# Optimization experiments

Measured on AMD Instinct MI355X. Metric: run time of the kernel, lower is better.

## Reference

```python
import jax, jax.numpy as jnp
import numpy as np

# ---- Cl(3,0) Cayley table: blade order [1, e1, e2, e3, e12, e13, e23, e123] ----
_IDX2BM = [0, 1, 2, 4, 3, 5, 6, 7]
_BM2IDX = {b: i for i, b in enumerate(_IDX2BM)}

def _blade_mul(i, j):
    a, b = _IDX2BM[i], _IDX2BM[j]
    s, aa = 0, a >> 1
    while aa:
        s += bin(aa & b).count('1')
        aa >>= 1
    return _BM2IDX[a ^ b], (-1) ** s

_pairs = [(i, j) + _blade_mul(i, j) for i in range(8) for j in range(8) if i != j]
_pairs = [(i, j, k, s) for (i, j, k, s) in _pairs if k != i and k != j]
SRC_I = np.array([p[0] for p in _pairs])  # (42,)
SRC_J = np.array([p[1] for p in _pairs])
TGT   = np.array([p[2] for p in _pairs])
SIGN  = np.array([p[3] for p in _pairs], dtype=np.float32)

ROPE_THETA = 10000.0


def _rope_tables(T, D, dtype):
    inv_freq = 1.0 / (ROPE_THETA ** (jnp.arange(0, D, 2, dtype=jnp.float32) / D))
    freqs = jnp.arange(T, dtype=jnp.float32)[:, None] * inv_freq[None, :]  # (T, D/2)
    emb = jnp.concatenate([freqs, freqs], axis=-1)  # (T, D)
    return jnp.cos(emb).astype(dtype), jnp.sin(emb).astype(dtype)


def _rotate_half(x):
    x1, x2 = jnp.split(x, 2, axis=-1)
    return jnp.concatenate([-x2, x1], axis=-1)


def setup_inputs() -> dict:
    key = jax.random.key(0)
    k1, k2, k3 = jax.random.split(key, 3)
    B, T, N, D = 2, 2048, 8, 128
    d_model = N * D
    mv = jax.random.normal(k1, (B, T, N, D), dtype=jnp.float32)
    # nn.Linear weights, stored as (in, out) for x @ W; scaled like default init
    W_qkv = jax.random.normal(k2, (d_model, 3 * d_model), dtype=jnp.float32) / np.sqrt(d_model)
    W_o = jax.random.normal(k3, (d_model, d_model), dtype=jnp.float32) / np.sqrt(d_model)
    alpha = jnp.ones((8, 8), dtype=jnp.float32) * 0.01  # cayley_mix_init_scale
    return {"mv": mv, "W_qkv": W_qkv, "W_o": W_o, "alpha": alpha}


def reference(mv, W_qkv, W_o, alpha):
    B, T, N, D = mv.shape
    x_flat = mv.reshape(B, T, N * D)
    qkv = (x_flat @ W_qkv).reshape(B, T, 3, N, D)
    q, k, v = qkv[:, :, 0], qkv[:, :, 1], qkv[:, :, 2]  # (B, T, N, D)

    cos, sin = _rope_tables(T, D, mv.dtype)  # (T, D)
    cos = cos[None, :, None, :]
    sin = sin[None, :, None, :]
    q = q * cos + _rotate_half(q) * sin
    k = k * cos + _rotate_half(k) * sin

    # (B, N, T, D)
    q = q.transpose(0, 2, 1, 3)
    k = k.transpose(0, 2, 1, 3)
    v = v.transpose(0, 2, 1, 3)

    scale = 1.0 / jnp.sqrt(jnp.asarray(D, dtype=mv.dtype))
    scores = jnp.einsum('bntd,bnsd->bnts', q, k) * scale  # (B, N, T, T)
    causal = jnp.tril(jnp.ones((T, T), dtype=bool))
    scores = jnp.where(causal[None, None], scores, -jnp.inf)
    attn = jax.nn.softmax(scores, axis=-1)
    out = jnp.einsum('bnts,bnsd->bntd', attn, v)  # (B, N, T, D)

    out = out.transpose(0, 2, 1, 3).reshape(B, T, N * D)
    out = (out @ W_o).reshape(B, T, N, D)

    # Cayley cross-blade mixing
    si, sj, tgt = jnp.asarray(SRC_I), jnp.asarray(SRC_J), jnp.asarray(TGT)
    pair_w = alpha[si, sj] * jnp.asarray(SIGN)  # (42,)
    contrib = out[:, :, si, :] * out[:, :, sj, :] * pair_w[None, None, :, None]
    mixed = jnp.zeros_like(out).at[:, :, tgt, :].add(contrib)
    return out + mixed
```

## Files before the change

kernel.cpp:

```cpp
#include <hip/hip_runtime.h>
#include <stdint.h>


typedef __attribute__((ext_vector_type(8)))  __bf16 bf16x8;
typedef __attribute__((ext_vector_type(8)))  uint16_t u16x8;
typedef __attribute__((ext_vector_type(4)))  float  f32x4;

__device__ __forceinline__ uint16_t f2bf(float f) {
    uint32_t u = __float_as_uint(f);
    u += 0x7FFFu + ((u >> 16) & 1u);
    return (uint16_t)(u >> 16);
}
__device__ __forceinline__ float bf2f(uint16_t h) {
    return __uint_as_float(((uint32_t)h) << 16);
}

__device__ __forceinline__ void gload_lds16(const void* g, void* l) {
    __builtin_amdgcn_global_load_lds(
        (__attribute__((address_space(1))) void*)g,
        (__attribute__((address_space(3))) void*)l, 16, 0, 0);
}

__global__ __launch_bounds__(256) void k_prep(const float* __restrict__ mv,
                                              const float* __restrict__ Wqkv,
                                              const float* __restrict__ Wo,
                                              uint16_t* __restrict__ Xbf,
                                              uint16_t* __restrict__ Wqt,
                                              uint16_t* __restrict__ Wot,
                                              float* __restrict__ ct,
                                              float* __restrict__ st) {
    __shared__ uint16_t tile[64][65];
    const int bid = blockIdx.x;
    const int tid = threadIdx.x;
    if (bid < 4096) {
        int i = bid * 256 + tid;
        float4 v = ((const float4*)mv)[i];
        ((ushort4*)Xbf)[i] = make_ushort4(f2bf(v.x), f2bf(v.y), f2bf(v.z), f2bf(v.w));
    } else if (bid < 5120) {
        const float* W; uint16_t* Wt; int N, bx, by;
        if (bid < 4864) { W = Wqkv; Wt = Wqt; N = 3072;
                          int b2 = bid - 4096; bx = b2 % 48; by = b2 / 48; }
        else            { W = Wo;   Wt = Wot; N = 1024;
                          int b3 = bid - 4864; bx = b3 & 15; by = b3 >> 4; }
        const int k0 = by * 64, n0 = bx * 64;
        const int c = tid & 63, r4 = tid >> 6;
#pragma unroll
        for (int i = 0; i < 16; ++i) {
            int r = r4 + i * 4;
            tile[r][c] = f2bf(W[(size_t)(k0 + r) * N + n0 + c]);
        }
        __syncthreads();
#pragma unroll
        for (int i = 0; i < 16; ++i) {
            int r = r4 + i * 4;
            Wt[(size_t)(n0 + r) * 1024 + k0 + c] = tile[c][r];
        }
    } else {
        int i = (bid - 5120) * 256 + tid;
        int t = i >> 6, f = i & 63;
        float inv = expf(-(float)f * 0.14391156830441f);
        float ang = (float)t * inv;
        ct[i] = cosf(ang);
        st[i] = sinf(ang);
    }
}

__global__ __launch_bounds__(256) void k_gemmqkv(const uint16_t* __restrict__ A,
                                                 const uint16_t* __restrict__ Bt,
                                                 const float* __restrict__ ct,
                                                 const float* __restrict__ st,
                                                 uint16_t* __restrict__ Qr,
                                                 uint16_t* __restrict__ Kr,
                                                 uint16_t* __restrict__ Vt) {
    __shared__ __align__(16) char smem[33792];
    uint16_t* Atile = (uint16_t*)smem;
    uint16_t* Btile = (uint16_t*)(smem + 16384);
    const int lin = blockIdx.y * 24 + blockIdx.x;
    const int logical = (lin & 7) * 96 + (lin >> 3);
    const int bx = logical % 24;
    const int m0 = (logical / 24) << 7, n0 = bx << 7;
    const int sec = bx >> 3, head = bx & 7;
    const int tid = threadIdx.x;
    const int l = tid & 63, w = tid >> 6;
    const int lr = l & 15, lg = l >> 4;
    const int wm = (w >> 1) << 6, wn = (w & 1) << 6;
    const int K = 1024;

    f32x4 acc[4][4];
#pragma unroll
    for (int i = 0; i < 4; ++i)
#pragma unroll
        for (int j = 0; j < 4; ++j) acc[i][j] = (f32x4){0.f, 0.f, 0.f, 0.f};

    for (int kt = 0; kt < 16; ++kt) {
        const int k0 = kt << 6;
        __syncthreads();
#pragma unroll
        for (int c = 0; c < 8; ++c) {
            int idx = c * 256 + tid;
            if (idx < 1024) {
                int r = idx >> 3, c16 = idx & 7;
                int sc = c16 ^ (r & 7);
                gload_lds16(A + (size_t)(m0 + r) * K + k0 + sc * 8, Atile + idx * 8);
            } else {
                int i2 = idx - 1024;
                int r = i2 >> 3, c16 = i2 & 7;
                int sc = c16 ^ (r & 7);
                gload_lds16(Bt + (size_t)(n0 + r) * K + k0 + sc * 8, Btile + i2 * 8);
            }
        }
        __syncthreads();
#pragma unroll
        for (int kk = 0; kk < 2; ++kk) {
            bf16x8 af[4], bfv[4];
#pragma unroll
            for (int i = 0; i < 4; ++i) {
                int ra = wm + i * 16 + lr;
                af[i]  = *(const bf16x8*)((char*)Atile + ra * 128 +
                          ((kk * 64 + lg * 16) ^ ((ra & 7) << 4)));
                int rb = wn + i * 16 + lr;
                bfv[i] = *(const bf16x8*)((char*)Btile + rb * 128 +
                          ((kk * 64 + lg * 16) ^ ((rb & 7) << 4)));
            }
#pragma unroll
            for (int mi = 0; mi < 4; ++mi)
#pragma unroll
                for (int ni = 0; ni < 4; ++ni)
                    acc[mi][ni] = __builtin_amdgcn_mfma_f32_16x16x32_bf16(
                        af[mi], bfv[ni], acc[mi][ni], 0, 0, 0);
        }
    }

    __syncthreads();
    uint16_t (*Tl)[132] = (uint16_t(*)[132])smem;
#pragma unroll
    for (int mi = 0; mi < 4; ++mi)
#pragma unroll
        for (int ni = 0; ni < 4; ++ni)
#pragma unroll
            for (int r = 0; r < 4; ++r)
                Tl[wm + mi * 16 + lg * 4 + r][wn + ni * 16 + lr] =
                    f2bf(acc[mi][ni][r]);
    __syncthreads();

    const int b = m0 >> 11, t0 = m0 & 2047;
    const size_t hidx = (size_t)(b * 8 + head);
    if (sec < 2) {
        uint16_t* outp = (sec == 0 ? Qr : Kr) + (hidx * 2048 + t0) * 128;
#pragma unroll
        for (int it = 0; it < 8; ++it) {
            int lin2 = it * 256 + tid;
            int tr = lin2 >> 4, d0 = (lin2 & 15) * 4;
            ushort4 lo = *(const ushort4*)&Tl[tr][d0];
            ushort4 hi = *(const ushort4*)&Tl[tr][d0 + 64];
            float4 cv = *(const float4*)&ct[(size_t)(t0 + tr) * 64 + d0];
            float4 sv = *(const float4*)&st[(size_t)(t0 + tr) * 64 + d0];
            ushort4 o1, o2;
            o1.x = f2bf(bf2f(lo.x) * cv.x - bf2f(hi.x) * sv.x);
            o2.x = f2bf(bf2f(hi.x) * cv.x + bf2f(lo.x) * sv.x);
            o1.y = f2bf(bf2f(lo.y) * cv.y - bf2f(hi.y) * sv.y);
            o2.y = f2bf(bf2f(hi.y) * cv.y + bf2f(lo.y) * sv.y);
            o1.z = f2bf(bf2f(lo.z) * cv.z - bf2f(hi.z) * sv.z);
            o2.z = f2bf(bf2f(hi.z) * cv.z + bf2f(lo.z) * sv.z);
            o1.w = f2bf(bf2f(lo.w) * cv.w - bf2f(hi.w) * sv.w);
            o2.w = f2bf(bf2f(hi.w) * cv.w + bf2f(lo.w) * sv.w);
            *(ushort4*)&outp[(size_t)tr * 128 + d0]      = o1;
            *(ushort4*)&outp[(size_t)tr * 128 + d0 + 64] = o2;
        }
    } else {
        uint16_t* vp = Vt + hidx * 128 * 2048;
#pragma unroll
        for (int it = 0; it < 8; ++it) {
            int lin2 = it * 256 + tid;
            int d = lin2 >> 4, tq = (lin2 & 15) * 8;
            ushort4 v0 = make_ushort4(Tl[tq + 0][d], Tl[tq + 1][d],
                                      Tl[tq + 2][d], Tl[tq + 3][d]);
            ushort4 v1 = make_ushort4(Tl[tq + 4][d], Tl[tq + 5][d],
                                      Tl[tq + 6][d], Tl[tq + 7][d]);
            *(ushort4*)&vp[(size_t)d * 2048 + t0 + tq]     = v0;
            *(ushort4*)&vp[(size_t)d * 2048 + t0 + tq + 4] = v1;
        }
    }
}

__global__ __launch_bounds__(256) void k_gemm2s(const uint16_t* __restrict__ A,
                                                const uint16_t* __restrict__ Bt,
                                                float* __restrict__ C) {
    __shared__ uint16_t Atile[128 * 64];
    __shared__ uint16_t Btile[64 * 64];
    const int kz = blockIdx.z;
    A  += (size_t)kz * 512;
    Bt += (size_t)kz * 512;
    C  += (size_t)kz * (4096u * 1024u);
    const int lin = blockIdx.y * 16 + blockIdx.x;
    const int logical = (lin & 7) * 64 + (lin >> 3);
    const int m0 = (logical >> 4) << 7, n0 = (logical & 15) << 6;
    const int tid = threadIdx.x;
    const int l = tid & 63, w = tid >> 6;
    const int lr = l & 15, lg = l >> 4;
    const int wm = (w >> 1) << 6, wn = (w & 1) << 5;

    f32x4 acc[4][2];
#pragma unroll
    for (int i = 0; i < 4; ++i)
#pragma unroll
        for (int j = 0; j < 2; ++j) acc[i][j] = (f32x4){0.f, 0.f, 0.f, 0.f};

    for (int kt = 0; kt < 8; ++kt) {
        const int k0 = kt << 6;
        __syncthreads();
#pragma unroll
        for (int c = 0; c < 6; ++c) {
            int idx = c * 256 + tid;
            if (idx < 1024) {
                int r = idx >> 3, c16 = idx & 7;
                int sc = c16 ^ (r & 7);
                gload_lds16(A + (size_t)(m0 + r) * 1024 + k0 + sc * 8, Atile + idx * 8);
            } else {
                int i2 = idx - 1024;
                int r = i2 >> 3, c16 = i2 & 7;
                int sc = c16 ^ (r & 7);
                gload_lds16(Bt + (size_t)(n0 + r) * 1024 + k0 + sc * 8, Btile + i2 * 8);
            }
        }
        __syncthreads();
#pragma unroll
        for (int kk = 0; kk < 2; ++kk) {
            bf16x8 af[4], bfv[2];
#pragma unroll
            for (int i = 0; i < 4; ++i) {
                int ra = wm + i * 16 + lr;
                af[i] = *(const bf16x8*)((char*)Atile + ra * 128 +
                         ((kk * 64 + lg * 16) ^ ((ra & 7) << 4)));
            }
#pragma unroll
            for (int j = 0; j < 2; ++j) {
                int rb = wn + j * 16 + lr;
                bfv[j] = *(const bf16x8*)((char*)Btile + rb * 128 +
                          ((kk * 64 + lg * 16) ^ ((rb & 7) << 4)));
            }
#pragma unroll
            for (int mi = 0; mi < 4; ++mi)
#pragma unroll
                for (int ni = 0; ni < 2; ++ni)
                    acc[mi][ni] = __builtin_amdgcn_mfma_f32_16x16x32_bf16(
                        af[mi], bfv[ni], acc[mi][ni], 0, 0, 0);
        }
    }
#pragma unroll
    for (int mi = 0; mi < 4; ++mi)
#pragma unroll
        for (int ni = 0; ni < 2; ++ni)
#pragma unroll
            for (int r = 0; r < 4; ++r) {
                int row = m0 + wm + mi * 16 + lg * 4 + r;
                int col = n0 + wn + ni * 16 + lr;
                C[(size_t)row * 1024 + col] = acc[mi][ni][r];
            }
}

__global__ __launch_bounds__(256) void k_attn(const uint16_t* __restrict__ Qg,
                                              const uint16_t* __restrict__ Kg,
                                              const uint16_t* __restrict__ Vtg,
                                              uint16_t* __restrict__ pbuf,
                                              float* __restrict__ mlg) {
    __shared__ uint16_t Klds[2][64 * 128];
    __shared__ uint16_t Vlds[2][128 * 64];
    __shared__ uint16_t Plds[4][16 * 64];

    const int h = blockIdx.x;
    int sy = blockIdx.y, qt = 31, ci = 0;
    for (int q = 31; q >= 0; --q) {
        int nc = (q + 8) >> 3;
        if (sy < nc) { qt = q; ci = sy; break; }
        sy -= nc;
    }
    const int slot = h * 80 + blockIdx.y;
    const int p0 = ci * 8;
    const int pend = min(p0 + 8, qt + 1);
    const int q0 = qt * 64;
    const int tid = threadIdx.x;
    const int l = tid & 63, w = tid >> 6;
    const int lr = l & 15, lg = l >> 4;
    const size_t headTD = (size_t)h * (2048 * 128);
    const uint16_t* Kh = Kg + headTD;
    const uint16_t* Vh = Vtg + headTD;

    bf16x8 qf[4];
    {
        const uint16_t* qp = Qg + headTD + (size_t)(q0 + w * 16 + lr) * 128 + lg * 8;
#pragma unroll
        for (int kc = 0; kc < 4; ++kc) qf[kc] = *(const bf16x8*)(qp + kc * 32);
    }

    f32x4 accO[8];
#pragma unroll
    for (int i = 0; i < 8; ++i) accO[i] = (f32x4){0.f, 0.f, 0.f, 0.f};
    float mrun = -1e30f, lrun = 0.f;

    const float SL2E = 0.08838834764831845f * 1.4426950408889634f;
    const int   swz  = (lr & 7) << 4;
    uint16_t* Pw = &Plds[w][0];

    auto STAGE = [&](int buf, int k0) {
#pragma unroll
        for (int p = 0; p < 4; ++p) {
            int u = p * 256 + tid;
            int row = u >> 4;
            int c16 = (u & 15) ^ (row & 7);
            gload_lds16(Kh + (size_t)(k0 + row) * 128 + c16 * 8,
                        (char*)&Klds[buf][0] + u * 16);
        }
#pragma unroll
        for (int p = 0; p < 4; ++p) {
            int u = p * 256 + tid;
            int d = u >> 3;
            int c8 = (u & 7) ^ (d & 7);
            gload_lds16(Vh + (size_t)d * 2048 + k0 + c8 * 8,
                        (char*)&Vlds[buf][0] + u * 16);
        }
    };

    STAGE(0, p0 * 64);

    for (int kt = p0; kt < pend; ++kt) {
        asm volatile("s_waitcnt vmcnt(0)" ::: "memory");
        __builtin_amdgcn_s_barrier();
        __builtin_amdgcn_sched_barrier(0);
        if (kt + 1 < pend) STAGE((kt + 1) & 1, (kt + 1) * 64);

        const char* Kb = (const char*)&Klds[kt & 1][0];
        const char* Vb = (const char*)&Vlds[kt & 1][0];

        float sv[4][4];
        __builtin_amdgcn_s_setprio(1);
#pragma unroll
        for (int cg = 0; cg < 4; ++cg) {
            f32x4 a = (f32x4){0.f, 0.f, 0.f, 0.f};
#pragma unroll
            for (int kc = 0; kc < 4; ++kc) {
                int kb = (cg * 16 + lr) * 256 + ((kc * 64 + lg * 16) ^ swz);
                bf16x8 kf = *(const bf16x8*)(Kb + kb);
                a = __builtin_amdgcn_mfma_f32_16x16x32_bf16(kf, qf[kc], a, 0, 0, 0);
            }
#pragma unroll
            for (int r = 0; r < 4; ++r) sv[cg][r] = a[r];
        }
        __builtin_amdgcn_s_setprio(0);

        if (kt == qt) {
#pragma unroll
            for (int cg = 0; cg < 4; ++cg)
#pragma unroll
                for (int r = 0; r < 4; ++r)
                    if (cg * 16 + lg * 4 + r > w * 16 + lr) sv[cg][r] = -1e30f;
        }

        float pml = sv[0][0];
#pragma unroll
        for (int cg = 0; cg < 4; ++cg)
#pragma unroll
            for (int r = 0; r < 4; ++r) pml = fmaxf(pml, sv[cg][r]);

        if (!__all(pml * SL2E <= mrun + 11.f)) {
            float mx = pml;
            mx = fmaxf(mx, __shfl_xor(mx, 16, 64));
            mx = fmaxf(mx, __shfl_xor(mx, 32, 64));
            float mn = fmaxf(mrun, mx * SL2E);
            float corr = exp2f(mrun - mn);
            mrun = mn;
            lrun *= corr;
            float ca[4];
#pragma unroll
            for (int r = 0; r < 4; ++r)
                ca[r] = __shfl(corr, (lg << 4) + lg * 4 + r, 64);
#pragma unroll
            for (int i = 0; i < 8; ++i)
#pragma unroll
                for (int r = 0; r < 4; ++r) accO[i][r] *= ca[r];
        }

        float psum = 0.f;
        float p[4][4];
#pragma unroll
        for (int cg = 0; cg < 4; ++cg)
#pragma unroll
            for (int r = 0; r < 4; ++r) {
                p[cg][r] = exp2f(fmaf(sv[cg][r], SL2E, -mrun));
                psum += p[cg][r];
            }
        lrun += psum;

#pragma unroll
        for (int cg = 0; cg < 4; ++cg) {
            uint32_t w0, w1;
            asm("v_cvt_pk_bf16_f32 %0, %1, %2" : "=v"(w0) : "v"(p[cg][0]), "v"(p[cg][1]));
            asm("v_cvt_pk_bf16_f32 %0, %1, %2" : "=v"(w1) : "v"(p[cg][2]), "v"(p[cg][3]));
            uint2 pr; pr.x = w0; pr.y = w1;
            *(uint2*)((char*)Pw + lr * 128 + ((cg * 32 + lg * 8) ^ swz)) = pr;
        }

        asm volatile("" ::: "memory");
        bf16x8 pf[2];
#pragma unroll
        for (int c = 0; c < 2; ++c)
            pf[c] = *(const bf16x8*)((char*)Pw + lr * 128 + ((c * 64 + lg * 16) ^ swz));

        __builtin_amdgcn_s_setprio(1);
#pragma unroll
        for (int ni = 0; ni < 8; ++ni)
#pragma unroll
            for (int c = 0; c < 2; ++c) {
                int vb = (ni * 16 + lr) * 128 + ((c * 64 + lg * 16) ^ swz);
                bf16x8 vf = *(const bf16x8*)(Vb + vb);
                accO[ni] = __builtin_amdgcn_mfma_f32_16x16x32_bf16(pf[c], vf, accO[ni], 0, 0, 0);
            }
        __builtin_amdgcn_s_setprio(0);
    }

    float lsum = lrun;
    lsum += __shfl_xor(lsum, 16, 64);
    lsum += __shfl_xor(lsum, 32, 64);
    uint16_t* pb = pbuf + (size_t)slot * 8192;
#pragma unroll
    for (int ni = 0; ni < 8; ++ni)
#pragma unroll
        for (int r = 0; r < 4; ++r) {
            int row = w * 16 + lg * 4 + r;
            pb[row * 128 + ni * 16 + lr] = f2bf(accO[ni][r]);
        }
    if (lg == 0) {
        mlg[slot * 128 + w * 16 + lr]      = mrun;
        mlg[slot * 128 + 64 + w * 16 + lr] = lsum;
    }
}

__global__ __launch_bounds__(256) void k_amerge(const uint16_t* __restrict__ pbuf,
                                                const float* __restrict__ mlg,
                                                uint16_t* __restrict__ AOg) {
    const int h = blockIdx.x, qt = blockIdx.y;
    int base = 0;
    for (int q = 31; q > qt; --q) base += (q + 8) >> 3;
    const int nc = (qt + 8) >> 3;
    const int slot0 = h * 80 + base;
    const int tid = threadIdx.x;
    const int row = tid >> 2, dq = (tid & 3) * 32;

    float M = -1e30f;
    for (int ci = 0; ci < nc; ++ci)
        M = fmaxf(M, mlg[(slot0 + ci) * 128 + row]);
    float L = 0.f;
    float o[32];
#pragma unroll
    for (int j = 0; j < 32; ++j) o[j] = 0.f;
    for (int ci = 0; ci < nc; ++ci) {
        int sl = slot0 + ci;
        float wgt = exp2f(mlg[sl * 128 + row] - M);
        L += mlg[sl * 128 + 64 + row] * wgt;
        const u16x8* pv = (const u16x8*)(pbuf + (size_t)sl * 8192 + row * 128 + dq);
#pragma unroll
        for (int jj = 0; jj < 4; ++jj) {
            u16x8 v = pv[jj];
#pragma unroll
            for (int k = 0; k < 8; ++k) o[jj * 8 + k] += bf2f(v[k]) * wgt;
        }
    }
    float inv = 1.f / L;
    const int b = h >> 3, n = h & 7;
    uint16_t* op = AOg + ((size_t)(b * 2048 + qt * 64 + row)) * 1024 + n * 128 + dq;
#pragma unroll
    for (int jj = 0; jj < 4; ++jj) {
        u16x8 v;
#pragma unroll
        for (int k = 0; k < 8; ++k) v[k] = f2bf(o[jj * 8 + k] * inv);
        ((u16x8*)op)[jj] = v;
    }
}

__global__ __launch_bounds__(256) void k_mix(const float* __restrict__ out0,
                                             const float* __restrict__ out1,
                                             const float* __restrict__ alpha,
                                             float* __restrict__ fin) {
    constexpr int SI[42] = {1,1,1,1,1,1, 2,2,2,2,2,2, 3,3,3,3,3,3, 4,4,4,4,4,4,
                            5,5,5,5,5,5, 6,6,6,6,6,6, 7,7,7,7,7,7};
    constexpr int SJ[42] = {2,3,4,5,6,7, 1,3,4,5,6,7, 1,2,4,5,6,7, 1,2,3,5,6,7,
                            1,2,3,4,6,7, 1,2,3,4,5,7, 1,2,3,4,5,6};
    constexpr int TG[42] = {4,5,2,3,7,6, 4,6,1,7,3,5, 5,6,7,1,2,4, 2,1,7,6,5,3,
                            3,7,1,6,4,2, 7,3,2,5,4,1, 6,5,4,3,2,1};
    constexpr float SG[42] = {+1,+1,+1,+1,+1,+1, -1,+1,-1,-1,+1,-1, -1,-1,+1,-1,-1,+1,
                              -1,+1,+1,-1,+1,-1, -1,-1,+1,+1,-1,+1, +1,-1,+1,-1,+1,-1,
                              +1,-1,+1,-1,+1,-1};
    int idx = blockIdx.x * 256 + threadIdx.x;
    int dq = (idx & 31) * 4, bt = idx >> 5;
    size_t base = (size_t)bt * 1024 + dq;
    float4 o[8], r[8];
#pragma unroll
    for (int hh = 0; hh < 8; ++hh) {
        float4 a = *(const float4*)&out0[base + hh * 128];
        float4 b = *(const float4*)&out1[base + hh * 128];
        o[hh] = make_float4(a.x + b.x, a.y + b.y, a.z + b.z, a.w + b.w);
        r[hh] = o[hh];
    }
#pragma unroll
    for (int p = 0; p < 42; ++p) {
        float wgt = alpha[SI[p] * 8 + SJ[p]] * SG[p];
        r[TG[p]].x += wgt * o[SI[p]].x * o[SJ[p]].x;
        r[TG[p]].y += wgt * o[SI[p]].y * o[SJ[p]].y;
        r[TG[p]].z += wgt * o[SI[p]].z * o[SJ[p]].z;
        r[TG[p]].w += wgt * o[SI[p]].w * o[SJ[p]].w;
    }
#pragma unroll
    for (int hh = 0; hh < 8; ++hh) *(float4*)&fin[base + hh * 128] = r[hh];
}

extern "C" void kernel_launch(void* const* d_in, const int* in_sizes, int n_in,
                              void* d_out, int out_size, void* d_ws, size_t ws_size,
                              hipStream_t stream) {
    (void)in_sizes; (void)n_in; (void)out_size; (void)ws_size;
    const float* mv    = (const float*)d_in[0];
    const float* Wqkv  = (const float*)d_in[1];
    const float* Wo    = (const float*)d_in[2];
    const float* alpha = (const float*)d_in[3];
    float* outp = (float*)d_out;
    char* ws = (char*)d_ws;

    uint16_t* Xbf  = (uint16_t*)(ws + 0);
    uint16_t* Wqt  = (uint16_t*)(ws + 8388608);
    uint16_t* Wot  = (uint16_t*)(ws + 14680064);
    uint16_t* Qr   = (uint16_t*)(ws + 41943040);
    uint16_t* Kr   = (uint16_t*)(ws + 50331648);
    uint16_t* Vt   = (uint16_t*)(ws + 58720256);
    float*    ctab = (float*)(ws + 67108864);
    float*    stab = (float*)(ws + 67633152);
    uint16_t* AO   = (uint16_t*)(ws + 0);
    float*    mlg  = (float*)(ws + 8388608);
    uint16_t* pbuf = (uint16_t*)(ws + 16777216);
    float*    outF0 = (float*)(ws + 16777216);
    float*    outF1 = (float*)(ws + 33554432);

    k_prep   <<<5632, 256, 0, stream>>>(mv, Wqkv, Wo, Xbf, Wqt, Wot, ctab, stab);
    k_gemmqkv<<<dim3(24, 32), 256, 0, stream>>>(Xbf, Wqt, ctab, stab, Qr, Kr, Vt);
    k_attn   <<<dim3(16, 80), 256, 0, stream>>>(Qr, Kr, Vt, pbuf, mlg);
    k_amerge <<<dim3(16, 32), 256, 0, stream>>>(pbuf, mlg, AO);
    k_gemm2s <<<dim3(16, 32, 2), 256, 0, stream>>>(AO, Wot, outF0);
    k_mix    <<<512, 256, 0, stream>>>(outF0, outF1, alpha, outp);
}
```

Measured before the change: 123.9 us.

## Single-buffer K/V staging in attention and write single-chunk tiles directly

The attention kernel drops double-buffered K/V LDS staging. Each iteration now loads its tile, waits, computes, and hits a trailing barrier, which roughly halves the kernel's LDS footprint so more blocks can be resident per CU. Query tiles with only one key chunk (qt <= 7) normalize and write straight into the AO buffer, so the merge kernel launches only for the remaining 24 tiles per head. The cost is lost overlap between global loads and MFMA work within a block, plus an extra barrier per iteration.

```diff
diff --git a/kernel.cpp b/kernel.cpp
--- a/kernel.cpp
+++ b/kernel.cpp
@@ -263,9 +263,10 @@
                                               const uint16_t* __restrict__ Kg,
                                               const uint16_t* __restrict__ Vtg,
                                               uint16_t* __restrict__ pbuf,
-                                              float* __restrict__ mlg) {
-    __shared__ uint16_t Klds[2][64 * 128];
-    __shared__ uint16_t Vlds[2][128 * 64];
+                                              float* __restrict__ mlg,
+                                              uint16_t* __restrict__ AOg) {
+    __shared__ uint16_t Klds[64 * 128];
+    __shared__ uint16_t Vlds[128 * 64];
     __shared__ uint16_t Plds[4][16 * 64];
 
     const int h = blockIdx.x;
@@ -302,14 +303,14 @@
     const int   swz  = (lr & 7) << 4;
     uint16_t* Pw = &Plds[w][0];
 
-    auto STAGE = [&](int buf, int k0) {
+    auto STAGE = [&](int k0) {
 #pragma unroll
         for (int p = 0; p < 4; ++p) {
             int u = p * 256 + tid;
             int row = u >> 4;
             int c16 = (u & 15) ^ (row & 7);
             gload_lds16(Kh + (size_t)(k0 + row) * 128 + c16 * 8,
-                        (char*)&Klds[buf][0] + u * 16);
+                        (char*)&Klds[0] + u * 16);
         }
 #pragma unroll
         for (int p = 0; p < 4; ++p) {
@@ -317,20 +318,18 @@
             int d = u >> 3;
             int c8 = (u & 7) ^ (d & 7);
             gload_lds16(Vh + (size_t)d * 2048 + k0 + c8 * 8,
-                        (char*)&Vlds[buf][0] + u * 16);
+                        (char*)&Vlds[0] + u * 16);
         }
     };
 
-    STAGE(0, p0 * 64);
-
     for (int kt = p0; kt < pend; ++kt) {
+        STAGE(kt * 64);
         asm volatile("s_waitcnt vmcnt(0)" ::: "memory");
         __builtin_amdgcn_s_barrier();
         __builtin_amdgcn_sched_barrier(0);
-        if (kt + 1 < pend) STAGE((kt + 1) & 1, (kt + 1) * 64);
-
-        const char* Kb = (const char*)&Klds[kt & 1][0];
-        const char* Vb = (const char*)&Vlds[kt & 1][0];
+
+        const char* Kb = (const char*)&Klds[0];
+        const char* Vb = (const char*)&Vlds[0];
 
         float sv[4][4];
         __builtin_amdgcn_s_setprio(1);
@@ -416,29 +415,49 @@
                 accO[ni] = __builtin_amdgcn_mfma_f32_16x16x32_bf16(pf[c], vf, accO[ni], 0, 0, 0);
             }
         __builtin_amdgcn_s_setprio(0);
+
+        __builtin_amdgcn_s_barrier();
     }
 
     float lsum = lrun;
     lsum += __shfl_xor(lsum, 16, 64);
     lsum += __shfl_xor(lsum, 32, 64);
-    uint16_t* pb = pbuf + (size_t)slot * 8192;
-#pragma unroll
-    for (int ni = 0; ni < 8; ++ni)
-#pragma unroll
-        for (int r = 0; r < 4; ++r) {
-            int row = w * 16 + lg * 4 + r;
-            pb[row * 128 + ni * 16 + lr] = f2bf(accO[ni][r]);
-        }
-    if (lg == 0) {
-        mlg[slot * 128 + w * 16 + lr]      = mrun;
-        mlg[slot * 128 + 64 + w * 16 + lr] = lsum;
+
+    if (qt <= 7) {
+        float linv = 1.f / lsum;
+        float inv[4];
+#pragma unroll
+        for (int r = 0; r < 4; ++r)
+            inv[r] = __shfl(linv, (lg << 4) + lg * 4 + r, 64);
+        const int b = h >> 3, n = h & 7;
+#pragma unroll
+        for (int ni = 0; ni < 8; ++ni)
+#pragma unroll
+            for (int r = 0; r < 4; ++r) {
+                int trow = q0 + w * 16 + lg * 4 + r;
+                AOg[((size_t)(b * 2048 + trow)) * 1024 + n * 128 + ni * 16 + lr] =
+                    f2bf(accO[ni][r] * inv[r]);
+            }
+    } else {
+        uint16_t* pb = pbuf + (size_t)slot * 8192;
+#pragma unroll
+        for (int ni = 0; ni < 8; ++ni)
+#pragma unroll
+            for (int r = 0; r < 4; ++r) {
+                int row = w * 16 + lg * 4 + r;
+                pb[row * 128 + ni * 16 + lr] = f2bf(accO[ni][r]);
+            }
+        if (lg == 0) {
+            mlg[slot * 128 + w * 16 + lr]      = mrun;
+            mlg[slot * 128 + 64 + w * 16 + lr] = lsum;
+        }
     }
 }
 
 __global__ __launch_bounds__(256) void k_amerge(const uint16_t* __restrict__ pbuf,
                                                 const float* __restrict__ mlg,
                                                 uint16_t* __restrict__ AOg) {
-    const int h = blockIdx.x, qt = blockIdx.y;
+    const int h = blockIdx.x, qt = 8 + blockIdx.y;
     int base = 0;
     for (int q = 31; q > qt; --q) base += (q + 8) >> 3;
     const int nc = (qt + 8) >> 3;
@@ -540,8 +559,8 @@
 
     k_prep   <<<5632, 256, 0, stream>>>(mv, Wqkv, Wo, Xbf, Wqt, Wot, ctab, stab);
     k_gemmqkv<<<dim3(24, 32), 256, 0, stream>>>(Xbf, Wqt, ctab, stab, Qr, Kr, Vt);
-    k_attn   <<<dim3(16, 80), 256, 0, stream>>>(Qr, Kr, Vt, pbuf, mlg);
-    k_amerge <<<dim3(16, 32), 256, 0, stream>>>(pbuf, mlg, AO);
+    k_attn   <<<dim3(16, 80), 256, 0, stream>>>(Qr, Kr, Vt, pbuf, mlg, AO);
+    k_amerge <<<dim3(16, 24), 256, 0, stream>>>(pbuf, mlg, AO);
     k_gemm2s <<<dim3(16, 32, 2), 256, 0, stream>>>(AO, Wot, outF0);
     k_mix    <<<512, 256, 0, stream>>>(outF0, outF1, alpha, outp);
 }
```

Result: faster. 120.3 us, median of 2 (-2.9%).
